# Kernel optimization log

Measured on AMD Instinct MI355X. Metric: run time of the kernel, lower is better.

Reference implementation:

```python
import jax, jax.numpy as jnp
import numpy as np

EPS = 1e-8

def setup_inputs() -> dict:
    key = jax.random.key(0)
    k1, k2, k3, k4 = jax.random.split(key, 4)
    b, in_c, out_c, style_c, k, h, w = 8, 512, 512, 512, 3, 64, 64
    return {
        "input": jax.random.normal(k1, (b, in_c, h, w), dtype=jnp.float32),
        "style": jax.random.normal(k2, (b, style_c), dtype=jnp.float32),
        "w_affine": jax.random.normal(k3, (in_c, style_c), dtype=jnp.float32),  # Linear weight, init N(0,1), runtime-scaled
        "b_affine": jnp.ones((1, in_c), dtype=jnp.float32),                     # Bias init_value=1.0
        "w_conv": jax.random.normal(k4, (out_c, in_c, k, k), dtype=jnp.float32),
    }

def reference(input, style, w_affine, b_affine, w_conv):
    b, in_c, h, w = input.shape
    out_c, _, kh, kw = w_conv.shape
    # Equalized-LR runtime scales (lr_mul=1):
    affine_scale = 1.0 / (w_affine.shape[1] ** 0.5)          # he_std for Linear
    conv_scale = 1.0 / ((in_c * kh * kw) ** 0.5)             # he_std for conv weight
    # affine: Linear + Bias (bias initialized to 1.0)
    s = style @ w_affine.T * affine_scale + b_affine          # [b, in_c]
    # modulate: per-sample weight tensor [b, out_c, in_c, kh, kw]
    wgt = s[:, None, :, None, None] * (w_conv * conv_scale)[None]
    # demodulate
    demod = jax.lax.rsqrt(jnp.sum(wgt * wgt, axis=(2, 3, 4), keepdims=True) + EPS)
    wgt = wgt * demod
    # grouped conv with groups = batch (stride=1, padding=1)
    x = input.reshape(1, b * in_c, h, w)
    wgt = wgt.reshape(b * out_c, in_c, kh, kw)
    out = jax.lax.conv_general_dilated(
        x, wgt,
        window_strides=(1, 1),
        padding=[(1, 1), (1, 1)],
        dimension_numbers=("NCHW", "OIHW", "NCHW"),
        feature_group_count=b,
    )
    return out.reshape(b, out_c, h, w)
```

## Files before the change

### kernel.cpp

```cpp
#include <hip/hip_runtime.h>
#include <hip/hip_bf16.h>

#define BB 8
#define CIN 512
#define COUT 512
#define HH 64
#define WW 64

#define AFF_SCALE 0.044194173824159216f
#define CONV_SCALE 0.014731391274719736f
#define CONV_SCALE2 (1.0f/4608.0f)

typedef short s16x8 __attribute__((ext_vector_type(8)));
typedef float f32x16 __attribute__((ext_vector_type(16)));

__device__ __forceinline__ unsigned short f2bf(float f) {
  __hip_bfloat16 h = __float2bfloat16(f);
  return *reinterpret_cast<unsigned short*>(&h);
}

__device__ __forceinline__ void gload_lds16(const void* g, void* l) {
  __builtin_amdgcn_global_load_lds(
      (const __attribute__((address_space(1))) unsigned int*)g,
      (__attribute__((address_space(3))) unsigned int*)l, 16, 0, 0);
}

__global__ __launch_bounds__(256) void affine_kernel(
    const float* __restrict__ style, const float* __restrict__ wa,
    const float* __restrict__ ba, float* __restrict__ smod) {
  int wid  = (blockIdx.x << 2) + (threadIdx.x >> 6);
  int lane = threadIdx.x & 63;
  int b  = wid >> 9;
  int ic = wid & 511;
  const float* s = style + b * CIN;
  const float* w = wa + (size_t)ic * CIN;
  float sum = 0.f;
#pragma unroll
  for (int k = 0; k < CIN / 64; ++k) sum += s[lane + 64 * k] * w[lane + 64 * k];
#pragma unroll
  for (int off = 32; off; off >>= 1) sum += __shfl_down(sum, off, 64);
  if (lane == 0) smod[wid] = sum * AFF_SCALE + ba[ic];
}

__global__ __launch_bounds__(256) void wsq_kernel(
    const float* __restrict__ wc, float* __restrict__ wsq) {
  int i = blockIdx.x * 256 + threadIdx.x;
  const float* p = wc + (size_t)i * 9;
  float s = 0.f;
#pragma unroll
  for (int k = 0; k < 9; ++k) { float v = p[k]; s += v * v; }
  wsq[i] = s;
}

__global__ __launch_bounds__(256) void demod_kernel(
    const float* __restrict__ smod, const float* __restrict__ wsq,
    float* __restrict__ demod) {
  int wid  = (blockIdx.x << 2) + (threadIdx.x >> 6);
  int lane = threadIdx.x & 63;
  int b  = wid >> 9;
  int oc = wid & 511;
  const float* s = smod + b * CIN;
  const float* w = wsq + (size_t)oc * CIN;
  float sum = 0.f;
#pragma unroll
  for (int k = 0; k < CIN / 64; ++k) {
    float sv = s[lane + 64 * k];
    sum += sv * sv * w[lane + 64 * k];
  }
#pragma unroll
  for (int off = 32; off; off >>= 1) sum += __shfl_down(sum, off, 64);
  if (lane == 0) demod[wid] = rsqrtf(sum * CONV_SCALE2 + 1e-8f) * CONV_SCALE;
}

__global__ __launch_bounds__(256) void premod_kernel(
    const float* __restrict__ xin, const float* __restrict__ smod,
    ushort* __restrict__ xt) {
  int n = blockIdx.x * 256 + threadIdx.x;
  int kg = n & 3;
  int x  = (n >> 2) & 63;
  int y  = (n >> 8) & 63;
  int g  = (n >> 14) & 15;
  int b  = n >> 18;
  int ic0 = g * 32 + kg * 8;
  const float* sp = smod + b * CIN + ic0;
  const float* xp = xin + (((size_t)b * CIN + ic0) * HH + y) * WW + x;
  s16x8 o;
#pragma unroll
  for (int j = 0; j < 8; ++j) {
    float v = xp[(size_t)j * HH * WW] * sp[j];
    o[j] = (short)f2bf(v);
  }
  *(s16x8*)(xt + (size_t)n * 8) = o;
}

__global__ __launch_bounds__(256) void wpack_kernel(
    const float* __restrict__ wc, ushort* __restrict__ wfrag) {
  int n = blockIdx.x * 256 + threadIdx.x;
  int l    = n & 63;
  int ks   = (n >> 6) & 1;
  int mf   = (n >> 7) & 15;
  int widx = n >> 11;
  int g = widx / 9, p = widx % 9;
  int kh = p % 3, kw = p / 3;
  int oc  = mf * 32 + (l & 31);
  int ic0 = g * 32 + ks * 16 + 8 * (l >> 5);
  s16x8 o;
#pragma unroll
  for (int j = 0; j < 8; ++j) {
    float v = wc[((size_t)oc * CIN + ic0 + j) * 9 + kh * 3 + kw];
    o[j] = (short)f2bf(v);
  }
  *(s16x8*)(wfrag + (size_t)n * 8) = o;
}

#define XS_ROW 4224
#define XS_BUF (6 * XS_ROW)
#define WS_BUFSZ 8192

#define MFMA1(A_, B_, C_) __builtin_amdgcn_mfma_f32_32x32x16_bf16(A_, B_, C_, 0, 0, 0)

#define MHK(KF, SX, SY) \
  __builtin_amdgcn_s_setprio(1); \
  acc[0][0] = MFMA1(wA[KF],     SX[0 + (KF)], acc[0][0]); \
  acc[1][0] = MFMA1(wA[2 + KF], SX[0 + (KF)], acc[1][0]); \
  acc[0][1] = MFMA1(wA[KF],     SX[2 + (KF)], acc[0][1]); \
  acc[1][1] = MFMA1(wA[2 + KF], SX[2 + (KF)], acc[1][1]); \
  acc[0][2] = MFMA1(wA[KF],     SY[0 + (KF)], acc[0][2]); \
  acc[1][2] = MFMA1(wA[2 + KF], SY[0 + (KF)], acc[1][2]); \
  acc[0][3] = MFMA1(wA[KF],     SY[2 + (KF)], acc[0][3]); \
  acc[1][3] = MFMA1(wA[2 + KF], SY[2 + (KF)], acc[1][3]); \
  __builtin_amdgcn_s_setprio(0);

#define LOADSLOT(S, RR, DXI) \
  S[0] = *(const s16x8*)(xs_r + (wr2 + (RR)) * XS_ROW + addrV[0][DXI][0]); \
  S[1] = *(const s16x8*)(xs_r + (wr2 + (RR)) * XS_ROW + addrV[0][DXI][1]); \
  S[2] = *(const s16x8*)(xs_r + (wr2 + (RR)) * XS_ROW + addrV[1][DXI][0]); \
  S[3] = *(const s16x8*)(xs_r + (wr2 + (RR)) * XS_ROW + addrV[1][DXI][1]);

#define ENTRYB \
  __builtin_amdgcn_sched_barrier(0); \
  asm volatile("s_waitcnt vmcnt(2) lgkmcnt(0)" ::: "memory"); \
  __builtin_amdgcn_sched_barrier(0); \
  __builtin_amdgcn_s_barrier(); \
  __builtin_amdgcn_sched_barrier(0);

#define AREAD(P) { \
  const char* wsp_ = wsL + ((P) % 3) * WS_BUFSZ + aoff; \
  wA[0] = *(const s16x8*)(wsp_); \
  wA[1] = *(const s16x8*)(wsp_ + 1024); \
  wA[2] = *(const s16x8*)(wsp_ + 2048); \
  wA[3] = *(const s16x8*)(wsp_ + 3072); }

#define WSISSUE(P) { \
  const char* ws_s = wsg + (size_t)((P) + 2) * 32768; \
  char* ws_d = wsdst + (((P) + 2) % 3) * WS_BUFSZ; \
  gload_lds16(ws_s, ws_d); \
  gload_lds16(ws_s + 4096, ws_d + 4096); }

#define GBODY(GG, TAILC) \
{ \
  const char* xs_r = (const char*)lds + (GG) * XS_BUF; \
  char* xs_w = lds + ((GG) ^ 1) * XS_BUF; \
  const char* wsg = wssrcb + (size_t)(g2 * 18 + (GG) * 9) * 32768; \
   ENTRYB AREAD(0) \
         LOADSLOT(bA, 0, 0) LOADSLOT(bB, 1, 0) \
         WSISSUE(0) \
         if (TAILC) stage6(xtb, (size_t)(b * 16 + g2 * 2 + (GG) + 1) * 262144, srcoff, xs_w, lds_woff, y0); \
         MHK(0, bA, bB) LOADSLOT(bC, 2, 0) MHK(1, bA, bB) \
   ENTRYB AREAD(1) WSISSUE(1) \
         MHK(0, bB, bC) LOADSLOT(bA, 3, 0) MHK(1, bB, bC) \
   ENTRYB AREAD(2) WSISSUE(2) \
         MHK(0, bC, bA) LOADSLOT(bB, 0, 1) MHK(1, bC, bA) LOADSLOT(bC, 1, 1) \
   ENTRYB AREAD(3) WSISSUE(3) \
         MHK(0, bB, bC) LOADSLOT(bA, 2, 1) MHK(1, bB, bC) \
   ENTRYB AREAD(4) WSISSUE(4) \
         MHK(0, bC, bA) LOADSLOT(bB, 3, 1) MHK(1, bC, bA) \
   ENTRYB AREAD(5) WSISSUE(5) \
         MHK(0, bA, bB) LOADSLOT(bC, 0, 2) MHK(1, bA, bB) LOADSLOT(bA, 1, 2) \
   ENTRYB AREAD(6) WSISSUE(6) \
         MHK(0, bC, bA) LOADSLOT(bB, 2, 2) MHK(1, bC, bA) \
   ENTRYB AREAD(7) WSISSUE(7) \
         MHK(0, bA, bB) LOADSLOT(bC, 3, 2) MHK(1, bA, bB) \
   ENTRYB AREAD(8) WSISSUE(8) \
         MHK(0, bB, bC) MHK(1, bB, bC) \
}

__device__ __forceinline__ void stage6(const char* xtb, size_t gbase, int srcoff,
                                       char* xs_w, int lds_woff, int y0) {
  __builtin_amdgcn_sched_barrier(0);
#pragma unroll
  for (int r = 0; r < 6; ++r) {
    int gy = y0 - 1 + r;
    if (gy >= 0 && gy < HH)
      gload_lds16(xtb + gbase + (size_t)gy * 4096 + srcoff,
                  xs_w + r * XS_ROW + lds_woff);
  }
  __builtin_amdgcn_sched_barrier(0);
}

__global__ __launch_bounds__(256, 2) void conv_mfma(
    const ushort* __restrict__ xt,
    const ushort* __restrict__ wfrag,
    const float* __restrict__ demod,
    float* __restrict__ out) {
  __shared__ char lds[2 * XS_BUF + 3 * WS_BUFSZ];

  int tid = threadIdx.x;
  int l = tid & 63, w = tid >> 6;
  int wm = w >> 1, wr = w & 1;
  int wr2 = wr * 2;
  int bid = blockIdx.x;
  int ocb = bid & 3;
  int b   = (bid >> 2) & 7;
  int yt  = bid >> 5;
  int y0  = yt * 4;

  const char* wsL = (const char*)lds + 2 * XS_BUF;
  char* wsdst = lds + 2 * XS_BUF + tid * 16;

  f32x16 acc[2][4];
#pragma unroll
  for (int i = 0; i < 2; ++i)
#pragma unroll
    for (int j = 0; j < 4; ++j)
#pragma unroll
      for (int e = 0; e < 16; ++e) acc[i][j][e] = 0.f;

  if (tid < 96) {
    int buf = tid & 1, side = (tid >> 1) & 1, kgz = (tid >> 2) & 3, r = tid >> 4;
    int chunk = side ? (260 + kgz) : kgz;
    *(int4*)(lds + buf * XS_BUF + r * XS_ROW + chunk * 16) = int4{0, 0, 0, 0};
  }
  if (y0 == 0) {
    for (int i = tid; i < 512; i += 256) {
      int buf = i & 1, chunk = 4 + (i >> 1);
      *(int4*)(lds + buf * XS_BUF + chunk * 16) = int4{0, 0, 0, 0};
    }
  }
  if (y0 == 60) {
    for (int i = tid; i < 512; i += 256) {
      int buf = i & 1, chunk = 4 + (i >> 1);
      *(int4*)(lds + buf * XS_BUF + 5 * XS_ROW + chunk * 16) = int4{0, 0, 0, 0};
    }
  }

  int addrV[2][3][2];
  {
    int lm = l & 31, kh2 = l >> 5;
#pragma unroll
    for (int ph = 0; ph < 2; ++ph)
#pragma unroll
      for (int dxi = 0; dxi < 3; ++dxi)
#pragma unroll
        for (int ks = 0; ks < 2; ++ks) {
          int col = ph * 32 + lm + dxi;
          int kg  = kh2 + 2 * ks;
          addrV[ph][dxi][ks] = (col * 4 + (kg ^ ((col >> 1) & 3))) * 16;
        }
  }

  int col_s = 1 + w * 16 + (l >> 2);
  int srcoff = (col_s - 1) * 64 + ((l & 3) ^ ((col_s >> 1) & 3)) * 16;
  int lds_woff = 64 + w * 1024;

  const char* xtb = (const char*)xt;
  const char* wssrcb = (const char*)wfrag + (size_t)ocb * 8192 + (size_t)tid * 16;
  int aoff = wm * 4096 + l * 16;

  {
    size_t gbase = (size_t)(b * 16) * 262144;
#pragma unroll
    for (int r = 0; r < 6; ++r) {
      int gy = y0 - 1 + r;
      if (gy >= 0 && gy < HH)
        gload_lds16(xtb + gbase + (size_t)gy * 4096 + srcoff,
                    lds + r * XS_ROW + lds_woff);
    }
    gload_lds16(wssrcb,          wsdst);
    gload_lds16(wssrcb + 4096,   wsdst + 4096);
    gload_lds16(wssrcb + 32768,        wsdst + WS_BUFSZ);
    gload_lds16(wssrcb + 32768 + 4096, wsdst + WS_BUFSZ + 4096);
  }

  s16x8 wA[4];
  s16x8 bA[4], bB[4], bC[4];

  for (int g2 = 0; g2 < 8; ++g2) {
    GBODY(0, true)
    GBODY(1, (g2 < 7))
  }

  int gy_base = y0 + wr2;
  int colbase = l & 31;
  int rowadd = 4 * (l >> 5);
#pragma unroll
  for (int q = 0; q < 2; ++q) {
#pragma unroll
    for (int reg = 0; reg < 16; ++reg) {
      int row = (reg & 3) + 8 * (reg >> 2) + rowadd;
      int oc = ocb * 128 + (wm * 2 + q) * 32 + row;
      float dm = demod[b * COUT + oc];
#pragma unroll
      for (int n = 0; n < 4; ++n) {
        int gy = gy_base + (n >> 1);
        int px = (n & 1) * 32 + colbase;
        out[((size_t)(b * COUT + oc)) * 4096 + gy * 64 + px] = acc[q][n][reg] * dm;
      }
    }
  }
}

extern "C" void kernel_launch(void* const* d_in, const int* in_sizes, int n_in,
                              void* d_out, int out_size, void* d_ws, size_t ws_size,
                              hipStream_t stream) {
  const float* input = (const float*)d_in[0];
  const float* style = (const float*)d_in[1];
  const float* wa    = (const float*)d_in[2];
  const float* ba    = (const float*)d_in[3];
  const float* wconv = (const float*)d_in[4];
  float* out = (float*)d_out;

  float* smod  = (float*)d_ws;
  float* demod = smod + BB * CIN;
  float* wsq   = demod + BB * COUT;
  ushort* wfrag = (ushort*)(wsq + (size_t)COUT * CIN);
  ushort* xt    = wfrag + (size_t)16 * 9 * 32 * 64 * 8;

  affine_kernel<<<BB * CIN / 4, 256, 0, stream>>>(style, wa, ba, smod);
  wsq_kernel<<<COUT * CIN / 256, 256, 0, stream>>>(wconv, wsq);
  demod_kernel<<<BB * COUT / 4, 256, 0, stream>>>(smod, wsq, demod);
  wpack_kernel<<<16 * 9 * 32 * 64 / 256, 256, 0, stream>>>(wconv, wfrag);
  premod_kernel<<<BB * 16 * 64 * 64 * 4 / 256, 256, 0, stream>>>(input, smod, xt);
  conv_mfma<<<BB * 4 * 16, 256, 0, stream>>>(xt, wfrag, demod, out);
}
```

Before: 152.3 us.

## Merge prep kernels into two launches and retime input staging in conv pipeline

Folds five preprocessing kernels into two launches by branching on block index, which removes launch overhead and inter-kernel gaps. In the conv main loop, the next input slab's stage is moved later, to phase 6 of each group. Out-of-range rows now always issue a load into an LDS trash row, so the vmcnt wait counts stay constant (vmcnt(8) for the later phases). A peeled last group drains with vmcnt(0). This adds a small amount of LDS and redundant loads for boundary tiles, and shortens the overlap window for input staging.

```diff
diff --git a/kernel.cpp b/kernel.cpp
--- a/kernel.cpp
+++ b/kernel.cpp
@@ -25,92 +25,91 @@
       (__attribute__((address_space(3))) unsigned int*)l, 16, 0, 0);
 }
 
-__global__ __launch_bounds__(256) void affine_kernel(
+__global__ __launch_bounds__(256) void prep1_kernel(
     const float* __restrict__ style, const float* __restrict__ wa,
-    const float* __restrict__ ba, float* __restrict__ smod) {
-  int wid  = (blockIdx.x << 2) + (threadIdx.x >> 6);
-  int lane = threadIdx.x & 63;
-  int b  = wid >> 9;
-  int ic = wid & 511;
-  const float* s = style + b * CIN;
-  const float* w = wa + (size_t)ic * CIN;
-  float sum = 0.f;
-#pragma unroll
-  for (int k = 0; k < CIN / 64; ++k) sum += s[lane + 64 * k] * w[lane + 64 * k];
-#pragma unroll
-  for (int off = 32; off; off >>= 1) sum += __shfl_down(sum, off, 64);
-  if (lane == 0) smod[wid] = sum * AFF_SCALE + ba[ic];
-}
-
-__global__ __launch_bounds__(256) void wsq_kernel(
-    const float* __restrict__ wc, float* __restrict__ wsq) {
-  int i = blockIdx.x * 256 + threadIdx.x;
-  const float* p = wc + (size_t)i * 9;
-  float s = 0.f;
-#pragma unroll
-  for (int k = 0; k < 9; ++k) { float v = p[k]; s += v * v; }
-  wsq[i] = s;
-}
-
-__global__ __launch_bounds__(256) void demod_kernel(
+    const float* __restrict__ ba, float* __restrict__ smod,
+    const float* __restrict__ wc, float* __restrict__ wsq,
+    ushort* __restrict__ wfrag) {
+  int bb = blockIdx.x;
+  if (bb < 1024) {
+    int wid  = (bb << 2) + (threadIdx.x >> 6);
+    int lane = threadIdx.x & 63;
+    int b  = wid >> 9;
+    int ic = wid & 511;
+    const float* s = style + b * CIN;
+    const float* w = wa + (size_t)ic * CIN;
+    float sum = 0.f;
+#pragma unroll
+    for (int k = 0; k < CIN / 64; ++k) sum += s[lane + 64 * k] * w[lane + 64 * k];
+#pragma unroll
+    for (int off = 32; off; off >>= 1) sum += __shfl_down(sum, off, 64);
+    if (lane == 0) smod[wid] = sum * AFF_SCALE + ba[ic];
+  } else if (bb < 2048) {
+    int i = (bb - 1024) * 256 + threadIdx.x;
+    const float* p = wc + (size_t)i * 9;
+    float s = 0.f;
+#pragma unroll
+    for (int k = 0; k < 9; ++k) { float v = p[k]; s += v * v; }
+    wsq[i] = s;
+  } else {
+    int n = (bb - 2048) * 256 + threadIdx.x;
+    int l    = n & 63;
+    int ks   = (n >> 6) & 1;
+    int mf   = (n >> 7) & 15;
+    int widx = n >> 11;
+    int g = widx / 9, p = widx % 9;
+    int kh = p % 3, kw = p / 3;
+    int oc  = mf * 32 + (l & 31);
+    int ic0 = g * 32 + ks * 16 + 8 * (l >> 5);
+    s16x8 o;
+#pragma unroll
+    for (int j = 0; j < 8; ++j) {
+      float v = wc[((size_t)oc * CIN + ic0 + j) * 9 + kh * 3 + kw];
+      o[j] = (short)f2bf(v);
+    }
+    *(s16x8*)(wfrag + (size_t)n * 8) = o;
+  }
+}
+
+__global__ __launch_bounds__(256) void prep2_kernel(
     const float* __restrict__ smod, const float* __restrict__ wsq,
-    float* __restrict__ demod) {
-  int wid  = (blockIdx.x << 2) + (threadIdx.x >> 6);
-  int lane = threadIdx.x & 63;
-  int b  = wid >> 9;
-  int oc = wid & 511;
-  const float* s = smod + b * CIN;
-  const float* w = wsq + (size_t)oc * CIN;
-  float sum = 0.f;
-#pragma unroll
-  for (int k = 0; k < CIN / 64; ++k) {
-    float sv = s[lane + 64 * k];
-    sum += sv * sv * w[lane + 64 * k];
-  }
-#pragma unroll
-  for (int off = 32; off; off >>= 1) sum += __shfl_down(sum, off, 64);
-  if (lane == 0) demod[wid] = rsqrtf(sum * CONV_SCALE2 + 1e-8f) * CONV_SCALE;
-}
-
-__global__ __launch_bounds__(256) void premod_kernel(
-    const float* __restrict__ xin, const float* __restrict__ smod,
-    ushort* __restrict__ xt) {
-  int n = blockIdx.x * 256 + threadIdx.x;
-  int kg = n & 3;
-  int x  = (n >> 2) & 63;
-  int y  = (n >> 8) & 63;
-  int g  = (n >> 14) & 15;
-  int b  = n >> 18;
-  int ic0 = g * 32 + kg * 8;
-  const float* sp = smod + b * CIN + ic0;
-  const float* xp = xin + (((size_t)b * CIN + ic0) * HH + y) * WW + x;
-  s16x8 o;
-#pragma unroll
-  for (int j = 0; j < 8; ++j) {
-    float v = xp[(size_t)j * HH * WW] * sp[j];
-    o[j] = (short)f2bf(v);
-  }
-  *(s16x8*)(xt + (size_t)n * 8) = o;
-}
-
-__global__ __launch_bounds__(256) void wpack_kernel(
-    const float* __restrict__ wc, ushort* __restrict__ wfrag) {
-  int n = blockIdx.x * 256 + threadIdx.x;
-  int l    = n & 63;
-  int ks   = (n >> 6) & 1;
-  int mf   = (n >> 7) & 15;
-  int widx = n >> 11;
-  int g = widx / 9, p = widx % 9;
-  int kh = p % 3, kw = p / 3;
-  int oc  = mf * 32 + (l & 31);
-  int ic0 = g * 32 + ks * 16 + 8 * (l >> 5);
-  s16x8 o;
-#pragma unroll
-  for (int j = 0; j < 8; ++j) {
-    float v = wc[((size_t)oc * CIN + ic0 + j) * 9 + kh * 3 + kw];
-    o[j] = (short)f2bf(v);
-  }
-  *(s16x8*)(wfrag + (size_t)n * 8) = o;
+    float* __restrict__ demod,
+    const float* __restrict__ xin, ushort* __restrict__ xt) {
+  int bb = blockIdx.x;
+  if (bb < 1024) {
+    int wid  = (bb << 2) + (threadIdx.x >> 6);
+    int lane = threadIdx.x & 63;
+    int b  = wid >> 9;
+    int oc = wid & 511;
+    const float* s = smod + b * CIN;
+    const float* w = wsq + (size_t)oc * CIN;
+    float sum = 0.f;
+#pragma unroll
+    for (int k = 0; k < CIN / 64; ++k) {
+      float sv = s[lane + 64 * k];
+      sum += sv * sv * w[lane + 64 * k];
+    }
+#pragma unroll
+    for (int off = 32; off; off >>= 1) sum += __shfl_down(sum, off, 64);
+    if (lane == 0) demod[wid] = rsqrtf(sum * CONV_SCALE2 + 1e-8f) * CONV_SCALE;
+  } else {
+    int n = (bb - 1024) * 256 + threadIdx.x;
+    int kg = n & 3;
+    int x  = (n >> 2) & 63;
+    int y  = (n >> 8) & 63;
+    int g  = (n >> 14) & 15;
+    int b  = n >> 18;
+    int ic0 = g * 32 + kg * 8;
+    const float* sp = smod + b * CIN + ic0;
+    const float* xp = xin + (((size_t)b * CIN + ic0) * HH + y) * WW + x;
+    s16x8 o;
+#pragma unroll
+    for (int j = 0; j < 8; ++j) {
+      float v = xp[(size_t)j * HH * WW] * sp[j];
+      o[j] = (short)f2bf(v);
+    }
+    *(s16x8*)(xt + (size_t)n * 8) = o;
+  }
 }
 
 #define XS_ROW 4224
@@ -137,9 +136,23 @@
   S[2] = *(const s16x8*)(xs_r + (wr2 + (RR)) * XS_ROW + addrV[1][DXI][0]); \
   S[3] = *(const s16x8*)(xs_r + (wr2 + (RR)) * XS_ROW + addrV[1][DXI][1]);
 
-#define ENTRYB \
+#define ENTRYB2 \
   __builtin_amdgcn_sched_barrier(0); \
   asm volatile("s_waitcnt vmcnt(2) lgkmcnt(0)" ::: "memory"); \
+  __builtin_amdgcn_sched_barrier(0); \
+  __builtin_amdgcn_s_barrier(); \
+  __builtin_amdgcn_sched_barrier(0);
+
+#define ENTRYB8 \
+  __builtin_amdgcn_sched_barrier(0); \
+  asm volatile("s_waitcnt vmcnt(8) lgkmcnt(0)" ::: "memory"); \
+  __builtin_amdgcn_sched_barrier(0); \
+  __builtin_amdgcn_s_barrier(); \
+  __builtin_amdgcn_sched_barrier(0);
+
+#define ENTRYB0 \
+  __builtin_amdgcn_sched_barrier(0); \
+  asm volatile("s_waitcnt vmcnt(0) lgkmcnt(0)" ::: "memory"); \
   __builtin_amdgcn_sched_barrier(0); \
   __builtin_amdgcn_s_barrier(); \
   __builtin_amdgcn_sched_barrier(0);
@@ -157,43 +170,70 @@
   gload_lds16(ws_s, ws_d); \
   gload_lds16(ws_s + 4096, ws_d + 4096); }
 
-#define GBODY(GG, TAILC) \
+#define GBODY(GG) \
 { \
   const char* xs_r = (const char*)lds + (GG) * XS_BUF; \
   char* xs_w = lds + ((GG) ^ 1) * XS_BUF; \
   const char* wsg = wssrcb + (size_t)(g2 * 18 + (GG) * 9) * 32768; \
-   ENTRYB AREAD(0) \
+   ENTRYB2 AREAD(0) \
          LOADSLOT(bA, 0, 0) LOADSLOT(bB, 1, 0) \
          WSISSUE(0) \
-         if (TAILC) stage6(xtb, (size_t)(b * 16 + g2 * 2 + (GG) + 1) * 262144, srcoff, xs_w, lds_woff, y0); \
          MHK(0, bA, bB) LOADSLOT(bC, 2, 0) MHK(1, bA, bB) \
-   ENTRYB AREAD(1) WSISSUE(1) \
+   ENTRYB2 AREAD(1) WSISSUE(1) \
          MHK(0, bB, bC) LOADSLOT(bA, 3, 0) MHK(1, bB, bC) \
-   ENTRYB AREAD(2) WSISSUE(2) \
+   ENTRYB2 AREAD(2) WSISSUE(2) \
          MHK(0, bC, bA) LOADSLOT(bB, 0, 1) MHK(1, bC, bA) LOADSLOT(bC, 1, 1) \
-   ENTRYB AREAD(3) WSISSUE(3) \
+   ENTRYB2 AREAD(3) WSISSUE(3) \
          MHK(0, bB, bC) LOADSLOT(bA, 2, 1) MHK(1, bB, bC) \
-   ENTRYB AREAD(4) WSISSUE(4) \
+   ENTRYB2 AREAD(4) WSISSUE(4) \
          MHK(0, bC, bA) LOADSLOT(bB, 3, 1) MHK(1, bC, bA) \
-   ENTRYB AREAD(5) WSISSUE(5) \
+   ENTRYB2 AREAD(5) WSISSUE(5) \
          MHK(0, bA, bB) LOADSLOT(bC, 0, 2) MHK(1, bA, bB) LOADSLOT(bA, 1, 2) \
-   ENTRYB AREAD(6) WSISSUE(6) \
+   ENTRYB2 AREAD(6) WSISSUE(6) \
+         stage6(xtb, (size_t)(b * 16 + g2 * 2 + (GG) + 1) * 262144, srcoff, xs_w, trash, lds_woff, y0); \
          MHK(0, bC, bA) LOADSLOT(bB, 2, 2) MHK(1, bC, bA) \
-   ENTRYB AREAD(7) WSISSUE(7) \
+   ENTRYB8 AREAD(7) WSISSUE(7) \
          MHK(0, bA, bB) LOADSLOT(bC, 3, 2) MHK(1, bA, bB) \
-   ENTRYB AREAD(8) WSISSUE(8) \
+   ENTRYB8 AREAD(8) WSISSUE(8) \
          MHK(0, bB, bC) MHK(1, bB, bC) \
 }
 
+#define GBODY_LAST \
+{ \
+  const char* xs_r = (const char*)lds + XS_BUF; \
+  const char* wsg = wssrcb + (size_t)(7 * 18 + 9) * 32768; \
+   ENTRYB2 AREAD(0) \
+         LOADSLOT(bA, 0, 0) LOADSLOT(bB, 1, 0) \
+         WSISSUE(0) \
+         MHK(0, bA, bB) LOADSLOT(bC, 2, 0) MHK(1, bA, bB) \
+   ENTRYB2 AREAD(1) WSISSUE(1) \
+         MHK(0, bB, bC) LOADSLOT(bA, 3, 0) MHK(1, bB, bC) \
+   ENTRYB2 AREAD(2) WSISSUE(2) \
+         MHK(0, bC, bA) LOADSLOT(bB, 0, 1) MHK(1, bC, bA) LOADSLOT(bC, 1, 1) \
+   ENTRYB2 AREAD(3) WSISSUE(3) \
+         MHK(0, bB, bC) LOADSLOT(bA, 2, 1) MHK(1, bB, bC) \
+   ENTRYB2 AREAD(4) WSISSUE(4) \
+         MHK(0, bC, bA) LOADSLOT(bB, 3, 1) MHK(1, bC, bA) \
+   ENTRYB2 AREAD(5) WSISSUE(5) \
+         MHK(0, bA, bB) LOADSLOT(bC, 0, 2) MHK(1, bA, bB) LOADSLOT(bA, 1, 2) \
+   ENTRYB2 AREAD(6) WSISSUE(6) \
+         MHK(0, bC, bA) LOADSLOT(bB, 2, 2) MHK(1, bC, bA) \
+   ENTRYB0 AREAD(7) \
+         MHK(0, bA, bB) LOADSLOT(bC, 3, 2) MHK(1, bA, bB) \
+   ENTRYB0 AREAD(8) \
+         MHK(0, bB, bC) MHK(1, bB, bC) \
+}
+
 __device__ __forceinline__ void stage6(const char* xtb, size_t gbase, int srcoff,
-                                       char* xs_w, int lds_woff, int y0) {
+                                       char* xs_w, char* trash, int lds_woff, int y0) {
   __builtin_amdgcn_sched_barrier(0);
 #pragma unroll
   for (int r = 0; r < 6; ++r) {
     int gy = y0 - 1 + r;
-    if (gy >= 0 && gy < HH)
-      gload_lds16(xtb + gbase + (size_t)gy * 4096 + srcoff,
-                  xs_w + r * XS_ROW + lds_woff);
+    bool ok = (gy >= 0) && (gy < HH);
+    int gyc = ok ? gy : (gy < 0 ? 0 : HH - 1);
+    char* dst = ok ? (xs_w + r * XS_ROW + lds_woff) : (trash + lds_woff);
+    gload_lds16(xtb + gbase + (size_t)gyc * 4096 + srcoff, dst);
   }
   __builtin_amdgcn_sched_barrier(0);
 }
@@ -203,7 +243,7 @@
     const ushort* __restrict__ wfrag,
     const float* __restrict__ demod,
     float* __restrict__ out) {
-  __shared__ char lds[2 * XS_BUF + 3 * WS_BUFSZ];
+  __shared__ char lds[2 * XS_BUF + 3 * WS_BUFSZ + XS_ROW];
 
   int tid = threadIdx.x;
   int l = tid & 63, w = tid >> 6;
@@ -217,6 +257,7 @@
 
   const char* wsL = (const char*)lds + 2 * XS_BUF;
   char* wsdst = lds + 2 * XS_BUF + tid * 16;
+  char* trash = lds + 2 * XS_BUF + 3 * WS_BUFSZ;
 
   f32x16 acc[2][4];
 #pragma unroll
@@ -281,13 +322,19 @@
     gload_lds16(wssrcb + 32768,        wsdst + WS_BUFSZ);
     gload_lds16(wssrcb + 32768 + 4096, wsdst + WS_BUFSZ + 4096);
   }
+  __syncthreads();
 
   s16x8 wA[4];
   s16x8 bA[4], bB[4], bC[4];
 
-  for (int g2 = 0; g2 < 8; ++g2) {
-    GBODY(0, true)
-    GBODY(1, (g2 < 7))
+  for (int g2 = 0; g2 < 7; ++g2) {
+    GBODY(0)
+    GBODY(1)
+  }
+  {
+    const int g2 = 7;
+    GBODY(0)
+    GBODY_LAST
   }
 
   int gy_base = y0 + wr2;
@@ -326,10 +373,7 @@
   ushort* wfrag = (ushort*)(wsq + (size_t)COUT * CIN);
   ushort* xt    = wfrag + (size_t)16 * 9 * 32 * 64 * 8;
 
-  affine_kernel<<<BB * CIN / 4, 256, 0, stream>>>(style, wa, ba, smod);
-  wsq_kernel<<<COUT * CIN / 256, 256, 0, stream>>>(wconv, wsq);
-  demod_kernel<<<BB * COUT / 4, 256, 0, stream>>>(smod, wsq, demod);
-  wpack_kernel<<<16 * 9 * 32 * 64 / 256, 256, 0, stream>>>(wconv, wfrag);
-  premod_kernel<<<BB * 16 * 64 * 64 * 4 / 256, 256, 0, stream>>>(input, smod, xt);
+  prep1_kernel<<<3200, 256, 0, stream>>>(style, wa, ba, smod, wconv, wsq, wfrag);
+  prep2_kernel<<<9216, 256, 0, stream>>>(smod, wsq, demod, input, xt);
   conv_mfma<<<BB * 4 * 16, 256, 0, stream>>>(xt, wfrag, demod, out);
 }
```

After: 146.5 us. -3.8%, faster.
